# Kernel tuning notes

Measured on AMD Instinct MI355X. Metric: run time of the kernel, lower is better.

## Reference

```python
import jax, jax.numpy as jnp
import numpy as np

B, L, DIM, HID, DSSH, DSSN = 2, 4096, 1024, 4096, 512, 512


def _ln(x, w, b):
    # LayerNorm over last dim, eps=1e-5 (torch default)
    m = x.mean(-1, keepdims=True)
    v = ((x - m) ** 2).mean(-1, keepdims=True)
    return (x - m) * jax.lax.rsqrt(v + 1e-5) * w + b


def _dss(x, n2_w, n2_b, LR, LI, CR, CI, D):
    # x: [B, L, dss_hidden]
    Lseq = x.shape[-2]
    xn = _ln(x, n2_w, n2_b)
    Lam = (-jnp.exp(LR) + 1j * jnp.exp(LI)).astype(jnp.complex64)        # [N]
    t = jnp.arange(Lseq, dtype=jnp.float32)
    S = jnp.exp(Lam[:, None] * t[None, :])                               # [N, L]
    Cc = (CR + 1j * CI) * ((jnp.exp(Lam) - 1.0) / Lam)                   # [H, N]
    K = jnp.einsum('hn,nl->lh', Cc, S).real                              # [L, H]
    n2 = 2 * Lseq
    Kf = jnp.fft.rfft(K, n=n2, axis=-2)                                  # [L+1, H]
    uf = jnp.fft.rfft(xn, n=n2, axis=-2)                                 # [B, L+1, H]
    y = jnp.fft.irfft(uf * Kf, n=n2, axis=-2)[..., :Lseq, :]
    return y + D * xn


def setup_inputs() -> dict:
    key = jax.random.key(0)
    ks = jax.random.split(key, 12)
    s = lambda k, sh, sc=1.0: jax.random.normal(k, sh, jnp.float32) * sc
    return dict(
        idx=s(ks[0], (B, L, DIM)),
        n1_w=jnp.ones((DIM,), jnp.float32), n1_b=jnp.zeros((DIM,), jnp.float32),
        Wxg=s(ks[1], (DIM, HID), 0.02),
        Wdin=s(ks[2], (DIM, DSSH), 0.02),
        n2_w=jnp.ones((DSSH,), jnp.float32), n2_b=jnp.zeros((DSSH,), jnp.float32),
        LR=s(ks[3], (DSSN,)), LI=s(ks[4], (DSSN,)),
        CR=s(ks[5], (DSSH, DSSN), 0.1), CI=s(ks[6], (DSSH, DSSN), 0.1),
        D=s(ks[7], (DSSH,)),
        Wgate=s(ks[8], (DSSH, HID), 0.02),
        Wout=s(ks[9], (HID, DIM), 0.02), bout=jnp.zeros((DIM,), jnp.float32),
    )


def reference(idx, n1_w, n1_b, Wxg, Wdin, n2_w, n2_b, LR, LI, CR, CI, D, Wgate, Wout, bout):
    x = _ln(idx, n1_w, n1_b)
    xg = x @ Wxg                                            # [B, L, HID]
    d = _dss(x @ Wdin, n2_w, n2_b, LR, LI, CR, CI, D)       # [B, L, DSSH]
    g = d @ Wgate                                           # [B, L, HID]
    out = (g * xg) @ Wout + bout                            # dropout is identity in eval
    return out + idx
```

## Files before the change

### kernel.cpp

```cpp
#include <hip/hip_runtime.h>
#include <math.h>


typedef unsigned short u16;
typedef unsigned int u32;
typedef __attribute__((ext_vector_type(8))) __bf16 bf16x8;
typedef __attribute__((ext_vector_type(4))) float f32x4;
typedef __attribute__((ext_vector_type(4))) u32 u32x4;

__device__ __forceinline__ u16 f2bf(float f) {
  u32 u = __float_as_uint(f);
  u32 r = u + 0x7FFFu + ((u >> 16) & 1u);
  return (u16)(r >> 16);
}
__device__ __forceinline__ float bf2f(u16 h) { return __uint_as_float(((u32)h) << 16); }

__device__ __forceinline__ void trans_conv_body(
    int bid, const float* __restrict__ in, u16* __restrict__ out, int K, int N,
    float (*t)[33]) {
  int tx = threadIdx.x & 31, ty = threadIdx.x >> 5;
  int nb = N >> 5;
  int k0 = (bid / nb) << 5;
  int n0 = (bid % nb) << 5;
#pragma unroll
  for (int i = 0; i < 32; i += 8)
    t[ty + i][tx] = in[(size_t)(k0 + ty + i) * N + n0 + tx];
  __syncthreads();
#pragma unroll
  for (int i = 0; i < 32; i += 8)
    out[(size_t)(n0 + ty + i) * K + k0 + tx] = f2bf(t[tx][ty + i]);
}

__device__ __forceinline__ void ln1_body(
    int bid, const float* __restrict__ in, const float* __restrict__ gw,
    const float* __restrict__ gb, u16* __restrict__ outp, float* sbuf) {
  const int D = 1024;
  int tid = threadIdx.x;
  const float4* r4 = (const float4*)(in + (size_t)bid * D);
  float4 v = r4[tid];
  float s = v.x + v.y + v.z + v.w;
  float ss = fmaf(v.x, v.x, fmaf(v.y, v.y, fmaf(v.z, v.z, v.w * v.w)));
#pragma unroll
  for (int o = 32; o >= 1; o >>= 1) { s += __shfl_xor(s, o); ss += __shfl_xor(ss, o); }
  float* sa = sbuf;
  float* sb = sbuf + 8;
  if ((tid & 63) == 0) { sa[tid >> 6] = s; sb[tid >> 6] = ss; }
  __syncthreads();
  float S = sa[0] + sa[1] + sa[2] + sa[3];
  float SS = sb[0] + sb[1] + sb[2] + sb[3];
  float mean = S / (float)D;
  float var = SS / (float)D - mean * mean;
  float inv = rsqrtf(var + 1e-5f);
  float4 wv = ((const float4*)gw)[tid];
  float4 bv = ((const float4*)gb)[tid];
  ushort4 o;
  o.x = f2bf((v.x - mean) * inv * wv.x + bv.x);
  o.y = f2bf((v.y - mean) * inv * wv.y + bv.y);
  o.z = f2bf((v.z - mean) * inv * wv.z + bv.z);
  o.w = f2bf((v.w - mean) * inv * wv.w + bv.w);
  ((ushort4*)outp)[(size_t)bid * (D >> 2) + tid] = o;
}

__device__ __forceinline__ void kgen_c_body(
    int bid, const float* __restrict__ LR, const float* __restrict__ LI,
    const float* __restrict__ CR, const float* __restrict__ CI, u16* __restrict__ Ct) {
  int idx0 = bid * 256 + threadIdx.x;
  int h = idx0 >> 9, n = idx0 & 511;
  float eLR = expf(LR[n]), eLI = expf(LI[n]);
  float lre = -eLR, lim = eLI;
  float er = expf(lre);
  float c, s;
  sincosf(lim, &s, &c);
  float wr = er * c - 1.0f, wi = er * s;
  float den = lre * lre + lim * lim;
  float gr = (wr * lre + wi * lim) / den;
  float gi = (wi * lre - wr * lim) / den;
  float cr = CR[(size_t)h * 512 + n], ci = CI[(size_t)h * 512 + n];
  float ccr = cr * gr - ci * gi;
  float cci = cr * gi + ci * gr;
  Ct[(size_t)h * 1024 + n] = f2bf(ccr);
  Ct[(size_t)h * 1024 + 512 + n] = f2bf(-cci);
}

__device__ __forceinline__ void twfill_body(int bid, float4* __restrict__ twg4) {
  int j = bid * 256 + threadIdx.x;
  float t1 = -6.2831853071795864769f * (float)j / 8192.0f;
  float s1, c1, s2, c2;
  sincosf(t1, &s1, &c1);
  sincosf(2.0f * t1, &s2, &c2);
  twg4[j] = {c1, s1, c2, s2};
}

__device__ __forceinline__ void tab_body(
    int bid, const float* __restrict__ LR, const float* __restrict__ LI,
    double* __restrict__ aexp, double* __restrict__ fexp) {
  int n = bid * 256 + threadIdx.x;
  if (n < 512) {
    aexp[n] = exp((double)LR[n]);
    fexp[n] = exp((double)LI[n]) * 0.15915494309189533577;
  }
}

__device__ __forceinline__ void ln_stats_body(
    int bid, const u16* __restrict__ xdTb, float* __restrict__ meanv,
    float* __restrict__ invv, float* sbuf) {
  int lane = threadIdx.x & 63;
  int seg = threadIdx.x >> 6;
  int col = bid * 64 + lane;
  float s = 0.f, ss = 0.f;
  const u16* p = xdTb + (size_t)(seg * 128) * 8192 + col;
#pragma unroll 8
  for (int r = 0; r < 128; ++r) {
    float v = bf2f(p[(size_t)r * 8192]);
    s += v; ss = fmaf(v, v, ss);
  }
  float* sa = sbuf;
  float* sb = sbuf + 256;
  sa[seg * 64 + lane] = s; sb[seg * 64 + lane] = ss;
  __syncthreads();
  if (threadIdx.x < 64) {
    float S = sa[lane] + sa[64 + lane] + sa[128 + lane] + sa[192 + lane];
    float SS = sb[lane] + sb[64 + lane] + sb[128 + lane] + sb[192 + lane];
    float mean = S * (1.0f / 512.0f);
    float var = SS * (1.0f / 512.0f) - mean * mean;
    meanv[bid * 64 + lane] = mean;
    invv[bid * 64 + lane] = rsqrtf(var + 1e-5f);
  }
}

template <int MODE>
__device__ __forceinline__ void gemm128p_body(
    int bid0, int nwg, const u16* __restrict__ A, const u16* __restrict__ Bt,
    int M, int N, int K, float* Cf, u16* Cb,
    const float* __restrict__ bias, const float* __restrict__ res, u16* lds) {
  constexpr int BUF = 16384;
  const int tid = threadIdx.x;
  const int lane = tid & 63;
  const int w = tid >> 6;
  const int cpx = nwg >> 3;
  const int bid = (nwg & 7) ? bid0 : (bid0 & 7) * cpx + (bid0 >> 3);
  const int tiles_n = N >> 7;
  const int tm = (bid / tiles_n) << 7;
  const int tn = (bid % tiles_n) << 7;

  const int wm = w >> 1, wn = w & 1;
  const int lr = lane & 15;
  const int kq = lane >> 4;
  const int l7 = lane & 7;
  const int rsub = lane >> 3;
  const int sslot = (lane & 7) ^ rsub;
  const u16* gA = A + (size_t)(tm + w * 32 + rsub) * K + sslot * 8;
  const u16* gB = Bt + (size_t)(tn + w * 32 + rsub) * K + sslot * 8;
  auto ldsc = (__attribute__((address_space(3))) char*)lds;

#define STAGE128(kt, c)                                                                   \
  {                                                                                       \
    const size_t kof = (size_t)(kt) << 6;                                                 \
    _Pragma("unroll") for (int i = 0; i < 4; ++i) {                                       \
      u32 da = (u32)((c)*BUF + (w * 32 + i * 8) * 64) * 2u;                               \
      __builtin_amdgcn_global_load_lds(                                                   \
          (const __attribute__((address_space(1))) void*)(gA + (size_t)(i * 8) * K + kof),\
          (__attribute__((address_space(3))) void*)(ldsc + da), 16, 0, 0);                \
      __builtin_amdgcn_global_load_lds(                                                   \
          (const __attribute__((address_space(1))) void*)(gB + (size_t)(i * 8) * K + kof),\
          (__attribute__((address_space(3))) void*)(ldsc + da + 16384), 16, 0, 0);        \
    }                                                                                     \
  }

  f32x4 acc[4][4] = {};
  const int NT = K >> 6;

  STAGE128(0, 0);
  asm volatile("s_waitcnt vmcnt(0)" ::: "memory");
  __builtin_amdgcn_s_barrier();
  __builtin_amdgcn_sched_barrier(0);

  int cur = 0;
  for (int kt = 0; kt < NT; ++kt) {
    if (kt + 1 < NT) STAGE128(kt + 1, cur ^ 1);
    const u32 ab = (u32)cur * BUF;
#pragma unroll
    for (int ks = 0; ks < 2; ++ks) {
      const int slp = ((((ks << 2) | kq)) ^ l7) << 3;
      bf16x8 af[4], bv[4];
#pragma unroll
      for (int mi = 0; mi < 4; ++mi) {
        int ra = wm * 64 + mi * 16 + lr;
        af[mi] = *(const bf16x8*)&lds[ab + ra * 64 + slp];
      }
#pragma unroll
      for (int ni = 0; ni < 4; ++ni) {
        int rb = wn * 64 + ni * 16 + lr;
        bv[ni] = *(const bf16x8*)&lds[ab + 8192 + rb * 64 + slp];
      }
      __builtin_amdgcn_s_setprio(1);
#pragma unroll
      for (int mi = 0; mi < 4; ++mi)
#pragma unroll
        for (int ni = 0; ni < 4; ++ni)
          acc[mi][ni] = __builtin_amdgcn_mfma_f32_16x16x32_bf16(af[mi], bv[ni], acc[mi][ni], 0, 0, 0);
      __builtin_amdgcn_s_setprio(0);
    }
    asm volatile("s_waitcnt vmcnt(0)" ::: "memory");
    __builtin_amdgcn_s_barrier();
    __builtin_amdgcn_sched_barrier(0);
    cur ^= 1;
  }
#undef STAGE128

  float* lf = (float*)lds + w * (16 * 68);
  const int er = lane >> 2;
  const int ec = (lane & 3) << 4;
  const int gcol = tn + wn * 64 + ec;
#pragma unroll
  for (int mi = 0; mi < 4; ++mi) {
#pragma unroll
    for (int ni = 0; ni < 4; ++ni)
#pragma unroll
      for (int j = 0; j < 4; ++j)
        lf[(kq * 4 + j) * 68 + ni * 16 + lr] = acc[mi][ni][j];
    float v[16];
#pragma unroll
    for (int q = 0; q < 4; ++q)
      *(f32x4*)&v[q * 4] = *(const f32x4*)&lf[er * 68 + ec + q * 4];
    const int gr = tm + wm * 64 + mi * 16 + er;
    if (MODE == 3) {
      const float* rr = res + (size_t)gr * N + gcol;
      const float* br = bias + gcol;
      float* orr = Cf + (size_t)gr * N + gcol;
#pragma unroll
      for (int q = 0; q < 4; ++q) {
        f32x4 rv = *(const f32x4*)(rr + q * 4);
        f32x4 bv4 = *(const f32x4*)(br + q * 4);
        f32x4 ov;
        ov[0] = v[q * 4 + 0] + bv4[0] + rv[0];
        ov[1] = v[q * 4 + 1] + bv4[1] + rv[1];
        ov[2] = v[q * 4 + 2] + bv4[2] + rv[2];
        ov[3] = v[q * 4 + 3] + bv4[3] + rv[3];
        *(f32x4*)(orr + q * 4) = ov;
      }
    } else {
      u32 pk[8];
#pragma unroll
      for (int e = 0; e < 8; ++e)
        pk[e] = (u32)f2bf(v[2 * e]) | ((u32)f2bf(v[2 * e + 1]) << 16);
      u16* orr = Cb + (size_t)gr * N + gcol;
      *(u32x4*)orr = u32x4{pk[0], pk[1], pk[2], pk[3]};
      *(u32x4*)(orr + 8) = u32x4{pk[4], pk[5], pk[6], pk[7]};
    }
  }
}


__global__ __launch_bounds__(256) void mega1(
    const float* __restrict__ idxf, const float* __restrict__ n1w, const float* __restrict__ n1b,
    const float* __restrict__ Wxg, const float* __restrict__ Wdin,
    const float* __restrict__ Wgate, const float* __restrict__ Wout,
    u16* __restrict__ Wxg_t, u16* __restrict__ Wdin_t,
    u16* __restrict__ Wgate_t, u16* __restrict__ Wout_t,
    u16* __restrict__ xbf, float4* __restrict__ twg4,
    const float* __restrict__ LR, const float* __restrict__ LI,
    const float* __restrict__ CR, const float* __restrict__ CI,
    u16* __restrict__ Ct, double* __restrict__ aexp, double* __restrict__ fexp) {
  __shared__ __align__(16) char smem[4352];
  int b = (int)blockIdx.x;
  if (b < 8192) { ln1_body(b, idxf, n1w, n1b, xbf, (float*)smem); return; }
  b -= 8192;
  if (b < 4096) { trans_conv_body(b, Wxg, Wxg_t, 1024, 4096, (float(*)[33])smem); return; }
  b -= 4096;
  if (b < 4096) { trans_conv_body(b, Wout, Wout_t, 4096, 1024, (float(*)[33])smem); return; }
  b -= 4096;
  if (b < 2048) { trans_conv_body(b, Wgate, Wgate_t, 512, 4096, (float(*)[33])smem); return; }
  b -= 2048;
  if (b < 512) { trans_conv_body(b, Wdin, Wdin_t, 1024, 512, (float(*)[33])smem); return; }
  b -= 512;
  if (b < 1024) { kgen_c_body(b, LR, LI, CR, CI, Ct); return; }
  b -= 1024;
  if (b < 8) { twfill_body(b, twg4); return; }
  b -= 8;
  tab_body(b, LR, LI, aexp, fexp);
}

__global__ __launch_bounds__(256) void kgen_s2(
    const double* __restrict__ aexp, const double* __restrict__ fexp,
    u16* __restrict__ SRSI) {
  int idx0 = (int)blockIdx.x * 256 + threadIdx.x;
  int l = idx0 >> 10;
  int kk = idx0 & 1023;
  int n = kk & 511;
  double fl = fexp[n] * (double)l;
  float rev = (float)(fl - floor(fl));
  float tri = (kk < 512) ? __builtin_amdgcn_cosf(rev) : __builtin_amdgcn_sinf(rev);
  float al = (float)aexp[n] * (float)l;
  SRSI[idx0] = f2bf(expf(-al) * tri);
}

template <int MODE>
__global__ __launch_bounds__(256, 2) void gemm128p(
    const u16* __restrict__ A, const u16* __restrict__ Bt,
    int M, int N, int K,
    float* Cf, u16* Cb,
    const float* __restrict__ bias, const float* __restrict__ res) {
  __shared__ __align__(16) u16 lds[2 * 16384];
  gemm128p_body<MODE>((int)blockIdx.x, (int)gridDim.x, A, Bt, M, N, K, Cf, Cb, bias, res, lds);
}

__global__ __launch_bounds__(256, 2) void l3mix(
    const u16* __restrict__ Ct, const u16* __restrict__ SRSI, u16* __restrict__ KTb,
    const u16* __restrict__ xdTb, float* __restrict__ meanv, float* __restrict__ invv) {
  __shared__ __align__(16) u16 lds[2 * 16384];
  int b = (int)blockIdx.x;
  if (b < 128) {
    gemm128p_body<1>(b, 128, Ct, SRSI, 512, 4096, 1024, nullptr, KTb, nullptr, nullptr, lds);
  } else {
    ln_stats_body(b - 128, xdTb, meanv, invv, (float*)lds);
  }
}

__global__ __launch_bounds__(256) void trans_bf(
    const u16* __restrict__ in, u16* __restrict__ out, int R, int C) {
  __shared__ u16 t[32][34];
  int tx = threadIdx.x & 31, ty = threadIdx.x >> 5;
  int nb = C >> 5;
  int r0 = (blockIdx.x / nb) << 5;
  int c0 = (blockIdx.x % nb) << 5;
#pragma unroll
  for (int i = 0; i < 32; i += 8)
    t[ty + i][tx] = in[(size_t)(r0 + ty + i) * C + c0 + tx];
  __syncthreads();
#pragma unroll
  for (int i = 0; i < 32; i += 8)
    out[(size_t)(c0 + ty + i) * R + r0 + tx] = t[tx][ty + i];
}

__global__ __launch_bounds__(256, 2) void gemm_fuse2(
    const u16* __restrict__ A1, const u16* __restrict__ B1t, int K1,
    const u16* __restrict__ A2, const u16* __restrict__ B2t, int K2,
    int M, int N, u16* __restrict__ Cb) {
  constexpr int BUF = 16384;
  __shared__ __align__(16) u16 lds[2 * BUF];
  const int tid = threadIdx.x;
  const int lane = tid & 63;
  const int w = tid >> 6;
  const int nwg = (int)gridDim.x;
  const int cpx = nwg >> 3;
  const int bid = (nwg & 7) ? (int)blockIdx.x
                            : ((int)blockIdx.x & 7) * cpx + ((int)blockIdx.x >> 3);
  const int tiles_n = N >> 7;
  const int tm = (bid / tiles_n) << 7;
  const int tn = (bid % tiles_n) << 7;

  const int wm = w >> 1, wn = w & 1;
  const int lr = lane & 15;
  const int kq = lane >> 4;
  const int l7 = lane & 7;
  const int rsub = lane >> 3;
  const int sslot = (lane & 7) ^ rsub;
  auto ldsc = (__attribute__((address_space(3))) char*)lds;

  f32x4 acc1[4][4] = {};
  f32x4 acc2[4][4] = {};

#define STAGEF(gA, gB, K, kt, c)                                                          \
  {                                                                                       \
    const size_t kof = (size_t)(kt) << 6;                                                 \
    _Pragma("unroll") for (int i = 0; i < 4; ++i) {                                       \
      u32 da = (u32)((c)*BUF + (w * 32 + i * 8) * 64) * 2u;                               \
      __builtin_amdgcn_global_load_lds(                                                   \
          (const __attribute__((address_space(1))) void*)((gA) + (size_t)(i * 8) * (K) + kof), \
          (__attribute__((address_space(3))) void*)(ldsc + da), 16, 0, 0);                \
      __builtin_amdgcn_global_load_lds(                                                   \
          (const __attribute__((address_space(1))) void*)((gB) + (size_t)(i * 8) * (K) + kof), \
          (__attribute__((address_space(3))) void*)(ldsc + da + 16384), 16, 0, 0);        \
    }                                                                                     \
  }

#define KLOOP(gA, gB, K, ACC)                                                             \
  {                                                                                       \
    const int NT = (K) >> 6;                                                              \
    STAGEF(gA, gB, K, 0, 0);                                                              \
    asm volatile("s_waitcnt vmcnt(0)" ::: "memory");                                      \
    __builtin_amdgcn_s_barrier();                                                         \
    __builtin_amdgcn_sched_barrier(0);                                                    \
    int cur = 0;                                                                          \
    for (int kt = 0; kt < NT; ++kt) {                                                     \
      if (kt + 1 < NT) STAGEF(gA, gB, K, kt + 1, cur ^ 1);                                \
      const u32 ab = (u32)cur * BUF;                                                      \
      _Pragma("unroll") for (int ks = 0; ks < 2; ++ks) {                                  \
        const int slp = ((((ks << 2) | kq)) ^ l7) << 3;                                   \
        bf16x8 af[4], bv[4];                                                              \
        _Pragma("unroll") for (int mi = 0; mi < 4; ++mi) {                                \
          int ra = wm * 64 + mi * 16 + lr;                                                \
          af[mi] = *(const bf16x8*)&lds[ab + ra * 64 + slp];                              \
        }                                                                                 \
        _Pragma("unroll") for (int ni = 0; ni < 4; ++ni) {                                \
          int rb = wn * 64 + ni * 16 + lr;                                                \
          bv[ni] = *(const bf16x8*)&lds[ab + 8192 + rb * 64 + slp];                       \
        }                                                                                 \
        __builtin_amdgcn_s_setprio(1);                                                    \
        _Pragma("unroll") for (int mi = 0; mi < 4; ++mi)                                  \
          _Pragma("unroll") for (int ni = 0; ni < 4; ++ni)                                \
            ACC[mi][ni] = __builtin_amdgcn_mfma_f32_16x16x32_bf16(af[mi], bv[ni], ACC[mi][ni], 0, 0, 0); \
        __builtin_amdgcn_s_setprio(0);                                                    \
      }                                                                                   \
      asm volatile("s_waitcnt vmcnt(0)" ::: "memory");                                    \
      __builtin_amdgcn_s_barrier();                                                       \
      __builtin_amdgcn_sched_barrier(0);                                                  \
      cur ^= 1;                                                                           \
    }                                                                                     \
  }

  {
    const u16* gA = A1 + (size_t)(tm + w * 32 + rsub) * K1 + sslot * 8;
    const u16* gB = B1t + (size_t)(tn + w * 32 + rsub) * K1 + sslot * 8;
    KLOOP(gA, gB, K1, acc1);
  }
  {
    const u16* gA = A2 + (size_t)(tm + w * 32 + rsub) * K2 + sslot * 8;
    const u16* gB = B2t + (size_t)(tn + w * 32 + rsub) * K2 + sslot * 8;
    KLOOP(gA, gB, K2, acc2);
  }
#undef KLOOP
#undef STAGEF

#pragma unroll
  for (int mi = 0; mi < 4; ++mi)
#pragma unroll
    for (int ni = 0; ni < 4; ++ni)
#pragma unroll
      for (int j = 0; j < 4; ++j)
        acc1[mi][ni][j] *= acc2[mi][ni][j];

  float* lf = (float*)lds + w * (16 * 68);
  const int er = lane >> 2;
  const int ec = (lane & 3) << 4;
  const int gcol = tn + wn * 64 + ec;
#pragma unroll
  for (int mi = 0; mi < 4; ++mi) {
#pragma unroll
    for (int ni = 0; ni < 4; ++ni)
#pragma unroll
      for (int j = 0; j < 4; ++j)
        lf[(kq * 4 + j) * 68 + ni * 16 + lr] = acc1[mi][ni][j];
    float v[16];
#pragma unroll
    for (int q = 0; q < 4; ++q)
      *(f32x4*)&v[q * 4] = *(const f32x4*)&lf[er * 68 + ec + q * 4];
    const int gr = tm + wm * 64 + mi * 16 + er;
    u32 pk[8];
#pragma unroll
    for (int e = 0; e < 8; ++e)
      pk[e] = (u32)f2bf(v[2 * e]) | ((u32)f2bf(v[2 * e + 1]) << 16);
    u16* orr = Cb + (size_t)gr * N + gcol;
    *(u32x4*)orr = u32x4{pk[0], pk[1], pk[2], pk[3]};
    *(u32x4*)(orr + 8) = u32x4{pk[4], pk[5], pk[6], pk[7]};
  }
}

struct C2 { float x, y; };
__device__ __forceinline__ C2 cadd(C2 a, C2 b) { return {a.x + b.x, a.y + b.y}; }
__device__ __forceinline__ C2 csub(C2 a, C2 b) { return {a.x - b.x, a.y - b.y}; }
__device__ __forceinline__ C2 cmul(C2 a, C2 b) {
  return {a.x * b.x - a.y * b.y, a.x * b.y + a.y * b.x};
}
__device__ __forceinline__ C2 cmulni(C2 a) { return {a.y, -a.x}; }

__device__ __forceinline__ int swz(int a) {
  return a ^ ((a >> 7) & 15) ^ ((a >> 11) & 3) ^ ((a >> 2) & 8) ^ ((a >> 3) & 2) ^ ((a >> 4) & 4);
}

#define BR13(x) ((int)(__brev((u32)(x)) >> 19))
#define RS 0.70710678118654752f

__device__ __forceinline__ void dif4(C2& a, C2& b, C2& c, C2& d, float4 wv) {
  C2 w = {wv.x, wv.y}, wm = {wv.y, -wv.x}, w2 = {wv.z, wv.w};
  C2 a1 = cadd(a, c);
  C2 c1 = cmul(csub(a, c), w);
  C2 b1 = cadd(b, d);
  C2 d1 = cmul(csub(b, d), wm);
  a = cadd(a1, b1);
  b = cmul(csub(a1, b1), w2);
  c = cadd(c1, d1);
  d = cmul(csub(c1, d1), w2);
}
__device__ __forceinline__ void dit4(C2& a, C2& b, C2& c, C2& d, float4 wv) {
  C2 w = {wv.x, wv.y}, wm = {wv.y, -wv.x}, wa = {wv.z, wv.w};
  C2 t = cmul(wa, b);
  C2 a1 = cadd(a, t), b1 = csub(a, t);
  C2 u = cmul(wa, d);
  C2 c1 = cadd(c, u), d1 = csub(c, u);
  C2 v = cmul(w, c1);
  C2 xx = cmul(wm, d1);
  a = cadd(a1, v);
  c = csub(a1, v);
  b = cadd(b1, xx);
  d = csub(b1, xx);
}

template <int L>
__device__ __forceinline__ void dif16(C2* z, int tid, const float4* __restrict__ twg4) {
  const int Q = 1 << (L - 2);
  const int pos2 = tid & (Q - 1);
  const int i0 = ((tid >> (L - 2)) << (L + 2)) | pos2;
  int ad[16]; C2 x[16];
#pragma unroll
  for (int k = 0; k < 16; ++k) { ad[k] = swz(i0 + k * Q); x[k] = z[ad[k]]; }
#pragma unroll
  for (int r = 0; r < 4; ++r)
    dif4(x[r], x[r + 4], x[r + 8], x[r + 12], twg4[(pos2 + r * Q) << (11 - L)]);
  {
    float4 wv2 = twg4[pos2 << (13 - L)];
#pragma unroll
    for (int m = 0; m < 4; ++m)
      dif4(x[4 * m], x[4 * m + 1], x[4 * m + 2], x[4 * m + 3], wv2);
  }
#pragma unroll
  for (int k = 0; k < 16; ++k) z[ad[k]] = x[k];
}
template <int L>
__device__ __forceinline__ void dit16(C2* z, int tid, const float4* __restrict__ twg4) {
  const int Q = 1 << (L - 2);
  const int pos2 = tid & (Q - 1);
  const int i0 = ((tid >> (L - 2)) << (L + 2)) | pos2;
  int ad[16]; C2 x[16];
#pragma unroll
  for (int k = 0; k < 16; ++k) { ad[k] = swz(i0 + k * Q); x[k] = z[ad[k]]; }
  {
    float4 wv2 = twg4[pos2 << (13 - L)];
#pragma unroll
    for (int m = 0; m < 4; ++m)
      dit4(x[4 * m], x[4 * m + 1], x[4 * m + 2], x[4 * m + 3], wv2);
  }
#pragma unroll
  for (int r = 0; r < 4; ++r)
    dit4(x[r], x[r + 4], x[r + 8], x[r + 12], twg4[(pos2 + r * Q) << (11 - L)]);
#pragma unroll
  for (int k = 0; k < 16; ++k) z[ad[k]] = x[k];
}

template <int LOGM>
__device__ __forceinline__ void dif_pass(C2* z, int tid, const float4* __restrict__ twg4) {
  const int M4 = 1 << LOGM;
#pragma unroll
  for (int j = 0; j < 4; ++j) {
    int b = tid + j * 512;
    int pos = b & (M4 - 1);
    int i0 = ((b >> LOGM) << (LOGM + 2)) | pos;
    int ia = swz(i0), ib = swz(i0 + M4), ic = swz(i0 + 2 * M4), id = swz(i0 + 3 * M4);
    C2 a = z[ia], bb = z[ib], c = z[ic], d = z[id];
    float4 wv = twg4[pos << (11 - LOGM)];
    dif4(a, bb, c, d, wv);
    z[ia] = a; z[ib] = bb; z[ic] = c; z[id] = d;
  }
}

template <int LOGM>
__device__ __forceinline__ void dit_pass(C2* z, int tid, const float4* __restrict__ twg4) {
  const int M4 = 1 << LOGM;
#pragma unroll
  for (int j = 0; j < 4; ++j) {
    int b = tid + j * 512;
    int pos = b & (M4 - 1);
    int i0 = ((b >> LOGM) << (LOGM + 2)) | pos;
    int ia = swz(i0), ib = swz(i0 + M4), ic = swz(i0 + 2 * M4), id = swz(i0 + 3 * M4);
    C2 a = z[ia], bb = z[ib], c = z[ic], d = z[id];
    float4 wv = twg4[pos << (11 - LOGM)];
    dit4(a, bb, c, d, wv);
    z[ia] = a; z[ib] = bb; z[ic] = c; z[id] = d;
  }
}

__device__ __forceinline__ void dif_r8(C2* z, int tid) {
#pragma unroll
  for (int j = 0; j < 2; ++j) {
    int base = (tid + j * 512) << 3;
    int ad[8]; C2 x[8];
#pragma unroll
    for (int e = 0; e < 8; ++e) { ad[e] = swz(base + e); x[e] = z[ad[e]]; }
    C2 t;
    t = csub(x[0], x[4]); x[0] = cadd(x[0], x[4]); x[4] = t;
    t = csub(x[1], x[5]); x[1] = cadd(x[1], x[5]); x[5] = cmul(t, {RS, -RS});
    t = csub(x[2], x[6]); x[2] = cadd(x[2], x[6]); x[6] = cmulni(t);
    t = csub(x[3], x[7]); x[3] = cadd(x[3], x[7]); x[7] = cmul(t, {-RS, -RS});
    t = csub(x[0], x[2]); x[0] = cadd(x[0], x[2]); x[2] = t;
    t = csub(x[1], x[3]); x[1] = cadd(x[1], x[3]); x[3] = cmulni(t);
    t = csub(x[4], x[6]); x[4] = cadd(x[4], x[6]); x[6] = t;
    t = csub(x[5], x[7]); x[5] = cadd(x[5], x[7]); x[7] = cmulni(t);
    t = csub(x[0], x[1]); x[0] = cadd(x[0], x[1]); x[1] = t;
    t = csub(x[2], x[3]); x[2] = cadd(x[2], x[3]); x[3] = t;
    t = csub(x[4], x[5]); x[4] = cadd(x[4], x[5]); x[5] = t;
    t = csub(x[6], x[7]); x[6] = cadd(x[6], x[7]); x[7] = t;
#pragma unroll
    for (int e = 0; e < 8; ++e) z[ad[e]] = x[e];
  }
}

__device__ __forceinline__ void r8_fused(C2* z, int tid, const u32* __restrict__ kfr) {
#pragma unroll
  for (int j = 0; j < 2; ++j) {
    int base = (tid + j * 512) << 3;
    int ad[8]; C2 x[8];
#pragma unroll
    for (int e = 0; e < 8; ++e) { ad[e] = swz(base + e); x[e] = z[ad[e]]; }
    u32x4 k0 = *(const u32x4*)(kfr + base);
    u32x4 k1 = *(const u32x4*)(kfr + base + 4);
    u32 kw[8] = {k0[0], k0[1], k0[2], k0[3], k1[0], k1[1], k1[2], k1[3]};
    C2 t;
    t = csub(x[0], x[4]); x[0] = cadd(x[0], x[4]); x[4] = t;
    t = csub(x[1], x[5]); x[1] = cadd(x[1], x[5]); x[5] = cmul(t, {RS, -RS});
    t = csub(x[2], x[6]); x[2] = cadd(x[2], x[6]); x[6] = cmulni(t);
    t = csub(x[3], x[7]); x[3] = cadd(x[3], x[7]); x[7] = cmul(t, {-RS, -RS});
    t = csub(x[0], x[2]); x[0] = cadd(x[0], x[2]); x[2] = t;
    t = csub(x[1], x[3]); x[1] = cadd(x[1], x[3]); x[3] = cmulni(t);
    t = csub(x[4], x[6]); x[4] = cadd(x[4], x[6]); x[6] = t;
    t = csub(x[5], x[7]); x[5] = cadd(x[5], x[7]); x[7] = cmulni(t);
    t = csub(x[0], x[1]); x[0] = cadd(x[0], x[1]); x[1] = t;
    t = csub(x[2], x[3]); x[2] = cadd(x[2], x[3]); x[3] = t;
    t = csub(x[4], x[5]); x[4] = cadd(x[4], x[5]); x[5] = t;
    t = csub(x[6], x[7]); x[6] = cadd(x[6], x[7]); x[7] = t;
#pragma unroll
    for (int e = 0; e < 8; ++e) {
      C2 kf = {bf2f((u16)(kw[e] & 0xffffu)), bf2f((u16)(kw[e] >> 16))};
      C2 pr = cmul(x[e], kf);
      x[e] = {pr.x, -pr.y};
    }
    t = x[1]; x[1] = csub(x[0], t); x[0] = cadd(x[0], t);
    t = x[3]; x[3] = csub(x[2], t); x[2] = cadd(x[2], t);
    t = x[5]; x[5] = csub(x[4], t); x[4] = cadd(x[4], t);
    t = x[7]; x[7] = csub(x[6], t); x[6] = cadd(x[6], t);
    t = x[2];          x[2] = csub(x[0], t); x[0] = cadd(x[0], t);
    t = cmulni(x[3]);  x[3] = csub(x[1], t); x[1] = cadd(x[1], t);
    t = x[6];          x[6] = csub(x[4], t); x[4] = cadd(x[4], t);
    t = cmulni(x[7]);  x[7] = csub(x[5], t); x[5] = cadd(x[5], t);
    t = x[4];                    x[4] = csub(x[0], t); x[0] = cadd(x[0], t);
    t = cmul(x[5], {RS, -RS});   x[5] = csub(x[1], t); x[1] = cadd(x[1], t);
    t = cmulni(x[6]);            x[6] = csub(x[2], t); x[2] = cadd(x[2], t);
    t = cmul(x[7], {-RS, -RS});  x[7] = csub(x[3], t); x[3] = cadd(x[3], t);
#pragma unroll
    for (int e = 0; e < 8; ++e) z[ad[e]] = x[e];
  }
}

__global__ __launch_bounds__(512) void kfft2(
    const u16* __restrict__ KTb, const float4* __restrict__ twg4,
    u32* __restrict__ Kfb) {
  __shared__ C2 z[8192];
  const int g = blockIdx.x;
  const int t = threadIdx.x;
  const u16* k0r = KTb + ((size_t)(2 * g) << 12);
  const u16* k1r = KTb + ((size_t)(2 * g + 1) << 12);

  C2 x[16];
#pragma unroll
  for (int k = 0; k < 8; ++k) {
    int l = t + k * 512;
    x[k] = {bf2f(k0r[l]), bf2f(k1r[l])};
  }
#pragma unroll
  for (int k = 8; k < 16; ++k) x[k] = {0.f, 0.f};
#pragma unroll
  for (int r = 0; r < 4; ++r)
    dif4(x[r], x[r + 4], x[r + 8], x[r + 12], twg4[t + r * 512]);
  {
    float4 wv2 = twg4[t << 2];
#pragma unroll
    for (int m = 0; m < 4; ++m)
      dif4(x[4 * m], x[4 * m + 1], x[4 * m + 2], x[4 * m + 3], wv2);
  }
#pragma unroll
  for (int k = 0; k < 16; ++k) z[swz(t + k * 512)] = x[k];
  __syncthreads();

  dif16<7>(z, t, twg4);   __syncthreads();
  dif_pass<3>(z, t, twg4); __syncthreads();
  dif_r8(z, t);            __syncthreads();

  u32* o0 = Kfb + ((size_t)(2 * g) << 13);
  u32* o1 = Kfb + ((size_t)(2 * g + 1) << 13);
#pragma unroll
  for (int it = 0; it < 16; ++it) {
    int p = t + it * 512;
    int k = BR13(p);
    int km = (8192 - k) & 8191;
    int p2 = BR13(km);
    C2 Zk = z[swz(p)], Zm = z[swz(p2)];
    float f0r = 0.5f * (Zk.x + Zm.x), f0i = 0.5f * (Zk.y - Zm.y);
    float f1r = 0.5f * (Zk.y + Zm.y), f1i = 0.5f * (Zm.x - Zk.x);
    o0[p] = (u32)f2bf(f0r) | ((u32)f2bf(f0i) << 16);
    o1[p] = (u32)f2bf(f1r) | ((u32)f2bf(f1i) << 16);
  }
}

__global__ __launch_bounds__(512) void fft_conv4(
    const u16* __restrict__ xdTb, const u32* __restrict__ Kfb,
    const float* __restrict__ meanv, const float* __restrict__ invv,
    const float* __restrict__ n2w, const float* __restrict__ n2b,
    const float* __restrict__ Dv, const float4* __restrict__ twg4,
    u16* __restrict__ dT) {
  __shared__ C2 z[8192];
  const int h = blockIdx.x;
  const int t = threadIdx.x;
  const u16* xr = xdTb + ((size_t)h << 13);
  const float w2h = n2w[h], b2h = n2b[h], Dh = Dv[h];

  float xn0r[8], xn1r[8];
  C2 x[16];
#pragma unroll
  for (int k = 0; k < 8; ++k) {
    int l = t + k * 512;
    float x0 = bf2f(xr[l]);
    float x1 = bf2f(xr[4096 + l]);
    xn0r[k] = (x0 - meanv[l]) * invv[l] * w2h + b2h;
    xn1r[k] = (x1 - meanv[4096 + l]) * invv[4096 + l] * w2h + b2h;
    x[k] = {xn0r[k], xn1r[k]};
  }
#pragma unroll
  for (int k = 8; k < 16; ++k) x[k] = {0.f, 0.f};
#pragma unroll
  for (int r = 0; r < 4; ++r)
    dif4(x[r], x[r + 4], x[r + 8], x[r + 12], twg4[t + r * 512]);
  {
    float4 wv2 = twg4[t << 2];
#pragma unroll
    for (int m = 0; m < 4; ++m)
      dif4(x[4 * m], x[4 * m + 1], x[4 * m + 2], x[4 * m + 3], wv2);
  }
#pragma unroll
  for (int k = 0; k < 16; ++k) z[swz(t + k * 512)] = x[k];
  __syncthreads();

  dif16<7>(z, t, twg4);    __syncthreads();
  dif_pass<3>(z, t, twg4);  __syncthreads();
  r8_fused(z, t, Kfb + ((size_t)h << 13)); __syncthreads();
  dit_pass<3>(z, t, twg4);  __syncthreads();
  dit16<7>(z, t, twg4);     __syncthreads();

#pragma unroll
  for (int k = 0; k < 16; ++k) x[k] = z[swz(t + k * 512)];
  {
    float4 wv2 = twg4[t << 2];
#pragma unroll
    for (int m = 0; m < 4; ++m)
      dit4(x[4 * m], x[4 * m + 1], x[4 * m + 2], x[4 * m + 3], wv2);
  }
  const float sc = 1.0f / 8192.0f;
  u16* drow = dT + ((size_t)h << 13);
#pragma unroll
  for (int r = 0; r < 4; ++r) {
    float4 wv = twg4[t + r * 512];
    C2 w = {wv.x, wv.y}, wm = {wv.y, -wv.x}, wa = {wv.z, wv.w};
    C2 a = x[r], bb = x[r + 4], c = x[r + 8], d = x[r + 12];
    C2 tt = cmul(wa, bb);
    C2 a1 = cadd(a, tt), b1 = csub(a, tt);
    C2 u = cmul(wa, d);
    C2 c1 = cadd(c, u), d1 = csub(c, u);
    C2 olo = cadd(a1, cmul(w, c1));
    C2 ohi = cadd(b1, cmul(wm, d1));
    int l0 = t + r * 512;
    int l1 = t + (r + 4) * 512;
    drow[l0] = f2bf(fmaf(Dh, xn0r[r], olo.x * sc));
    drow[4096 + l0] = f2bf(fmaf(Dh, xn1r[r], -olo.y * sc));
    drow[l1] = f2bf(fmaf(Dh, xn0r[r + 4], ohi.x * sc));
    drow[4096 + l1] = f2bf(fmaf(Dh, xn1r[r + 4], -ohi.y * sc));
  }
}

extern "C" void kernel_launch(void* const* d_in, const int* in_sizes, int n_in,
                              void* d_out, int out_size, void* d_ws, size_t ws_size,
                              hipStream_t stream) {
  (void)in_sizes; (void)n_in; (void)out_size; (void)ws_size;
  const float* idx  = (const float*)d_in[0];
  const float* n1w  = (const float*)d_in[1];
  const float* n1b  = (const float*)d_in[2];
  const float* Wxg  = (const float*)d_in[3];
  const float* Wdin = (const float*)d_in[4];
  const float* n2w  = (const float*)d_in[5];
  const float* n2b  = (const float*)d_in[6];
  const float* LR   = (const float*)d_in[7];
  const float* LI   = (const float*)d_in[8];
  const float* CR   = (const float*)d_in[9];
  const float* CI   = (const float*)d_in[10];
  const float* Dv   = (const float*)d_in[11];
  const float* Wgate= (const float*)d_in[12];
  const float* Wout = (const float*)d_in[13];
  const float* bout = (const float*)d_in[14];
  float* out = (float*)d_out;

  const int L = 4096, DIM = 1024, HID = 4096, H = 512;
  const int M = 8192;

  char* p = (char*)d_ws;
  auto alloc = [&](size_t bytes) { char* q = p; p += (bytes + 255) & ~(size_t)255; return q; };
  u16* Wxg_t   = (u16*)alloc((size_t)HID * DIM * 2);
  u16* Wdin_t  = (u16*)alloc((size_t)H * DIM * 2);
  u16* Wgate_t = (u16*)alloc((size_t)HID * H * 2);
  u16* Wout_t  = (u16*)alloc((size_t)DIM * HID * 2);
  u16* xbf     = (u16*)alloc((size_t)M * DIM * 2);
  u16* ebuf    = (u16*)alloc((size_t)M * HID * 2);
  u16* xdTb    = (u16*)alloc((size_t)H * M * 2);
  float* meanv = (float*)alloc((size_t)M * 4);
  float* invv  = (float*)alloc((size_t)M * 4);
  u16* SRSI    = (u16*)alloc((size_t)L * 1024 * 2);
  u16* Ct      = (u16*)alloc((size_t)H * 1024 * 2);
  u16* KTb     = (u16*)alloc((size_t)H * L * 2);
  u16* dTm     = (u16*)alloc((size_t)H * M * 2);
  u16* dbuf    = (u16*)alloc((size_t)M * H * 2);
  float4* twg4 = (float4*)alloc((size_t)2048 * 16);
  u32* Kfb     = (u32*)alloc((size_t)H * M * 4);
  double* aexp = (double*)alloc((size_t)512 * 8);
  double* fexp = (double*)alloc((size_t)512 * 8);

  mega1<<<dim3(8192 + 4096 + 4096 + 2048 + 512 + 1024 + 8 + 2), 256, 0, stream>>>(
      idx, n1w, n1b, Wxg, Wdin, Wgate, Wout,
      Wxg_t, Wdin_t, Wgate_t, Wout_t, xbf, twg4, LR, LI, CR, CI, Ct, aexp, fexp);
  kgen_s2<<<dim3(L * 1024 / 256), 256, 0, stream>>>(aexp, fexp, SRSI);
  gemm128p<1><<<dim3((H / 128) * (M / 128)), 256, 0, stream>>>(
      Wdin_t, xbf, H, M, DIM, nullptr, xdTb, nullptr, nullptr);
  l3mix<<<dim3(256), 256, 0, stream>>>(Ct, SRSI, KTb, xdTb, meanv, invv);
  kfft2<<<dim3(H / 2), 512, 0, stream>>>(KTb, twg4, Kfb);
  fft_conv4<<<dim3(H), 512, 0, stream>>>(xdTb, Kfb, meanv, invv, n2w, n2b, Dv, twg4, dTm);
  trans_bf<<<dim3((H / 32) * (M / 32)), 256, 0, stream>>>(dTm, dbuf, H, M);
  gemm_fuse2<<<dim3((M / 128) * (HID / 128)), 256, 0, stream>>>(
      xbf, Wxg_t, DIM, dbuf, Wgate_t, H, M, HID, ebuf);
  gemm128p<3><<<dim3((M / 128) * (DIM / 128)), 256, 0, stream>>>(
      ebuf, Wout_t, M, DIM, HID, out, nullptr, bout, idx);
}
```

Measured before the change: 311.6 us.

## Replace double-buffered BK=64 GEMM mainloop with 4-stage BK=32 LDS ring

All GEMM mainloops (gemm128s, l3mix GEMM part, gemm_fuse2) now use a 4-deep ring of BK=32 stages loaded with global_load_lds. Partial vmcnt waits keep up to three stages in flight instead of draining all loads every iteration. The LDS swizzle is redone for 32-element rows. Each iteration now has two barriers and less MFMA work per sync, which adds synchronisation overhead in exchange for deeper memory latency hiding.

```diff
diff --git a/kernel.cpp b/kernel.cpp
--- a/kernel.cpp
+++ b/kernel.cpp
@@ -128,12 +128,61 @@
   }
 }
 
+
+#define RING_STAGE(AP, BP, K, kt)                                                         \
+  {                                                                                       \
+    const u32 cb = (u32)((kt) & 3) * 16384u;                                              \
+    const size_t kof = (size_t)(kt) << 5;                                                 \
+    _Pragma("unroll") for (int i = 0; i < 2; ++i) {                                       \
+      u32 da = cb + (u32)(i * 64 + wv16) * 64u;                                           \
+      __builtin_amdgcn_global_load_lds(                                                   \
+          (const __attribute__((address_space(1))) void*)((AP) + (size_t)(i * 64) * (K) + kof), \
+          (__attribute__((address_space(3))) void*)(ldsc + da), 16, 0, 0);                \
+      __builtin_amdgcn_global_load_lds(                                                   \
+          (const __attribute__((address_space(1))) void*)((BP) + (size_t)(i * 64) * (K) + kof), \
+          (__attribute__((address_space(3))) void*)(ldsc + da + 8192), 16, 0, 0);         \
+    }                                                                                     \
+  }
+
+#define RING_LOOP(Aptr, Bptr, K, ACC)                                                     \
+  {                                                                                       \
+    const int NT = (K) >> 5;                                                              \
+    RING_STAGE(Aptr, Bptr, K, 0);                                                         \
+    RING_STAGE(Aptr, Bptr, K, 1);                                                         \
+    RING_STAGE(Aptr, Bptr, K, 2);                                                         \
+    asm volatile("s_waitcnt vmcnt(8)" ::: "memory");                                      \
+    __builtin_amdgcn_s_barrier();                                                         \
+    for (int kt = 0; kt < NT; ++kt) {                                                     \
+      if (kt + 3 < NT) RING_STAGE(Aptr, Bptr, K, kt + 3);                                 \
+      if (kt + 3 < NT)      asm volatile("s_waitcnt vmcnt(12)" ::: "memory");             \
+      else if (kt + 2 < NT) asm volatile("s_waitcnt vmcnt(8)" ::: "memory");              \
+      else if (kt + 1 < NT) asm volatile("s_waitcnt vmcnt(4)" ::: "memory");              \
+      else                  asm volatile("s_waitcnt vmcnt(0)" ::: "memory");              \
+      __builtin_amdgcn_s_barrier();                                                       \
+      const u32 ab = (u32)(kt & 3) * 8192u;                                               \
+      bf16x8 af[4], bv[4];                                                                \
+      _Pragma("unroll") for (int mi = 0; mi < 4; ++mi) {                                  \
+        int ra = wm * 64 + mi * 16 + lr;                                                  \
+        af[mi] = *(const bf16x8*)&lds[ab + ra * 32 + slp];                                \
+      }                                                                                   \
+      _Pragma("unroll") for (int ni = 0; ni < 4; ++ni) {                                  \
+        int rb = wn * 64 + ni * 16 + lr;                                                  \
+        bv[ni] = *(const bf16x8*)&lds[ab + 4096 + rb * 32 + slp];                         \
+      }                                                                                   \
+      __builtin_amdgcn_s_setprio(1);                                                      \
+      _Pragma("unroll") for (int mi = 0; mi < 4; ++mi)                                    \
+        _Pragma("unroll") for (int ni = 0; ni < 4; ++ni)                                  \
+          ACC[mi][ni] = __builtin_amdgcn_mfma_f32_16x16x32_bf16(af[mi], bv[ni], ACC[mi][ni], 0, 0, 0); \
+      __builtin_amdgcn_s_setprio(0);                                                      \
+      __builtin_amdgcn_s_barrier();                                                      \
+    }                                                                                     \
+  }
+
 template <int MODE>
-__device__ __forceinline__ void gemm128p_body(
+__device__ __forceinline__ void gemm128s_body(
     int bid0, int nwg, const u16* __restrict__ A, const u16* __restrict__ Bt,
     int M, int N, int K, float* Cf, u16* Cb,
     const float* __restrict__ bias, const float* __restrict__ res, u16* lds) {
-  constexpr int BUF = 16384;
   const int tid = threadIdx.x;
   const int lane = tid & 63;
   const int w = tid >> 6;
@@ -146,67 +195,16 @@
   const int wm = w >> 1, wn = w & 1;
   const int lr = lane & 15;
   const int kq = lane >> 4;
-  const int l7 = lane & 7;
-  const int rsub = lane >> 3;
-  const int sslot = (lane & 7) ^ rsub;
-  const u16* gA = A + (size_t)(tm + w * 32 + rsub) * K + sslot * 8;
-  const u16* gB = Bt + (size_t)(tn + w * 32 + rsub) * K + sslot * 8;
+  const int slp = ((kq ^ (lr & 3)) << 3);
+  const int wv16 = w * 16;
+  const int srow = wv16 + (lane >> 2);
+  const int sslot = (lane & 3) ^ ((lane >> 2) & 3);
+  const u16* gA = A + (size_t)(tm + srow) * K + sslot * 8;
+  const u16* gB = Bt + (size_t)(tn + srow) * K + sslot * 8;
   auto ldsc = (__attribute__((address_space(3))) char*)lds;
 
-#define STAGE128(kt, c)                                                                   \
-  {                                                                                       \
-    const size_t kof = (size_t)(kt) << 6;                                                 \
-    _Pragma("unroll") for (int i = 0; i < 4; ++i) {                                       \
-      u32 da = (u32)((c)*BUF + (w * 32 + i * 8) * 64) * 2u;                               \
-      __builtin_amdgcn_global_load_lds(                                                   \
-          (const __attribute__((address_space(1))) void*)(gA + (size_t)(i * 8) * K + kof),\
-          (__attribute__((address_space(3))) void*)(ldsc + da), 16, 0, 0);                \
-      __builtin_amdgcn_global_load_lds(                                                   \
-          (const __attribute__((address_space(1))) void*)(gB + (size_t)(i * 8) * K + kof),\
-          (__attribute__((address_space(3))) void*)(ldsc + da + 16384), 16, 0, 0);        \
-    }                                                                                     \
-  }
-
   f32x4 acc[4][4] = {};
-  const int NT = K >> 6;
-
-  STAGE128(0, 0);
-  asm volatile("s_waitcnt vmcnt(0)" ::: "memory");
-  __builtin_amdgcn_s_barrier();
-  __builtin_amdgcn_sched_barrier(0);
-
-  int cur = 0;
-  for (int kt = 0; kt < NT; ++kt) {
-    if (kt + 1 < NT) STAGE128(kt + 1, cur ^ 1);
-    const u32 ab = (u32)cur * BUF;
-#pragma unroll
-    for (int ks = 0; ks < 2; ++ks) {
-      const int slp = ((((ks << 2) | kq)) ^ l7) << 3;
-      bf16x8 af[4], bv[4];
-#pragma unroll
-      for (int mi = 0; mi < 4; ++mi) {
-        int ra = wm * 64 + mi * 16 + lr;
-        af[mi] = *(const bf16x8*)&lds[ab + ra * 64 + slp];
-      }
-#pragma unroll
-      for (int ni = 0; ni < 4; ++ni) {
-        int rb = wn * 64 + ni * 16 + lr;
-        bv[ni] = *(const bf16x8*)&lds[ab + 8192 + rb * 64 + slp];
-      }
-      __builtin_amdgcn_s_setprio(1);
-#pragma unroll
-      for (int mi = 0; mi < 4; ++mi)
-#pragma unroll
-        for (int ni = 0; ni < 4; ++ni)
-          acc[mi][ni] = __builtin_amdgcn_mfma_f32_16x16x32_bf16(af[mi], bv[ni], acc[mi][ni], 0, 0, 0);
-      __builtin_amdgcn_s_setprio(0);
-    }
-    asm volatile("s_waitcnt vmcnt(0)" ::: "memory");
-    __builtin_amdgcn_s_barrier();
-    __builtin_amdgcn_sched_barrier(0);
-    cur ^= 1;
-  }
-#undef STAGE128
+  RING_LOOP(gA, gB, K, acc);
 
   float* lf = (float*)lds + w * (16 * 68);
   const int er = lane >> 2;
@@ -250,7 +248,6 @@
     }
   }
 }
-
 
 __global__ __launch_bounds__(256) void mega1(
     const float* __restrict__ idxf, const float* __restrict__ n1w, const float* __restrict__ n1b,
@@ -296,22 +293,22 @@
 }
 
 template <int MODE>
-__global__ __launch_bounds__(256, 2) void gemm128p(
+__global__ __launch_bounds__(256, 2) void gemm128s(
     const u16* __restrict__ A, const u16* __restrict__ Bt,
     int M, int N, int K,
     float* Cf, u16* Cb,
     const float* __restrict__ bias, const float* __restrict__ res) {
-  __shared__ __align__(16) u16 lds[2 * 16384];
-  gemm128p_body<MODE>((int)blockIdx.x, (int)gridDim.x, A, Bt, M, N, K, Cf, Cb, bias, res, lds);
+  __shared__ __align__(16) u16 lds[32768];
+  gemm128s_body<MODE>((int)blockIdx.x, (int)gridDim.x, A, Bt, M, N, K, Cf, Cb, bias, res, lds);
 }
 
 __global__ __launch_bounds__(256, 2) void l3mix(
     const u16* __restrict__ Ct, const u16* __restrict__ SRSI, u16* __restrict__ KTb,
     const u16* __restrict__ xdTb, float* __restrict__ meanv, float* __restrict__ invv) {
-  __shared__ __align__(16) u16 lds[2 * 16384];
+  __shared__ __align__(16) u16 lds[32768];
   int b = (int)blockIdx.x;
   if (b < 128) {
-    gemm128p_body<1>(b, 128, Ct, SRSI, 512, 4096, 1024, nullptr, KTb, nullptr, nullptr, lds);
+    gemm128s_body<1>(b, 128, Ct, SRSI, 512, 4096, 1024, nullptr, KTb, nullptr, nullptr, lds);
   } else {
     ln_stats_body(b - 128, xdTb, meanv, invv, (float*)lds);
   }
@@ -337,8 +334,7 @@
     const u16* __restrict__ A1, const u16* __restrict__ B1t, int K1,
     const u16* __restrict__ A2, const u16* __restrict__ B2t, int K2,
     int M, int N, u16* __restrict__ Cb) {
-  constexpr int BUF = 16384;
-  __shared__ __align__(16) u16 lds[2 * BUF];
+  __shared__ __align__(16) u16 lds[32768];
   const int tid = threadIdx.x;
   const int lane = tid & 63;
   const int w = tid >> 6;
@@ -353,75 +349,25 @@
   const int wm = w >> 1, wn = w & 1;
   const int lr = lane & 15;
   const int kq = lane >> 4;
-  const int l7 = lane & 7;
-  const int rsub = lane >> 3;
-  const int sslot = (lane & 7) ^ rsub;
+  const int slp = ((kq ^ (lr & 3)) << 3);
+  const int wv16 = w * 16;
+  const int srow = wv16 + (lane >> 2);
+  const int sslot = (lane & 3) ^ ((lane >> 2) & 3);
   auto ldsc = (__attribute__((address_space(3))) char*)lds;
 
   f32x4 acc1[4][4] = {};
   f32x4 acc2[4][4] = {};
 
-#define STAGEF(gA, gB, K, kt, c)                                                          \
-  {                                                                                       \
-    const size_t kof = (size_t)(kt) << 6;                                                 \
-    _Pragma("unroll") for (int i = 0; i < 4; ++i) {                                       \
-      u32 da = (u32)((c)*BUF + (w * 32 + i * 8) * 64) * 2u;                               \
-      __builtin_amdgcn_global_load_lds(                                                   \
-          (const __attribute__((address_space(1))) void*)((gA) + (size_t)(i * 8) * (K) + kof), \
-          (__attribute__((address_space(3))) void*)(ldsc + da), 16, 0, 0);                \
-      __builtin_amdgcn_global_load_lds(                                                   \
-          (const __attribute__((address_space(1))) void*)((gB) + (size_t)(i * 8) * (K) + kof), \
-          (__attribute__((address_space(3))) void*)(ldsc + da + 16384), 16, 0, 0);        \
-    }                                                                                     \
-  }
-
-#define KLOOP(gA, gB, K, ACC)                                                             \
-  {                                                                                       \
-    const int NT = (K) >> 6;                                                              \
-    STAGEF(gA, gB, K, 0, 0);                                                              \
-    asm volatile("s_waitcnt vmcnt(0)" ::: "memory");                                      \
-    __builtin_amdgcn_s_barrier();                                                         \
-    __builtin_amdgcn_sched_barrier(0);                                                    \
-    int cur = 0;                                                                          \
-    for (int kt = 0; kt < NT; ++kt) {                                                     \
-      if (kt + 1 < NT) STAGEF(gA, gB, K, kt + 1, cur ^ 1);                                \
-      const u32 ab = (u32)cur * BUF;                                                      \
-      _Pragma("unroll") for (int ks = 0; ks < 2; ++ks) {                                  \
-        const int slp = ((((ks << 2) | kq)) ^ l7) << 3;                                   \
-        bf16x8 af[4], bv[4];                                                              \
-        _Pragma("unroll") for (int mi = 0; mi < 4; ++mi) {                                \
-          int ra = wm * 64 + mi * 16 + lr;                                                \
-          af[mi] = *(const bf16x8*)&lds[ab + ra * 64 + slp];                              \
-        }                                                                                 \
-        _Pragma("unroll") for (int ni = 0; ni < 4; ++ni) {                                \
-          int rb = wn * 64 + ni * 16 + lr;                                                \
-          bv[ni] = *(const bf16x8*)&lds[ab + 8192 + rb * 64 + slp];                       \
-        }                                                                                 \
-        __builtin_amdgcn_s_setprio(1);                                                    \
-        _Pragma("unroll") for (int mi = 0; mi < 4; ++mi)                                  \
-          _Pragma("unroll") for (int ni = 0; ni < 4; ++ni)                                \
-            ACC[mi][ni] = __builtin_amdgcn_mfma_f32_16x16x32_bf16(af[mi], bv[ni], ACC[mi][ni], 0, 0, 0); \
-        __builtin_amdgcn_s_setprio(0);                                                    \
-      }                                                                                   \
-      asm volatile("s_waitcnt vmcnt(0)" ::: "memory");                                    \
-      __builtin_amdgcn_s_barrier();                                                       \
-      __builtin_amdgcn_sched_barrier(0);                                                  \
-      cur ^= 1;                                                                           \
-    }                                                                                     \
-  }
-
   {
-    const u16* gA = A1 + (size_t)(tm + w * 32 + rsub) * K1 + sslot * 8;
-    const u16* gB = B1t + (size_t)(tn + w * 32 + rsub) * K1 + sslot * 8;
-    KLOOP(gA, gB, K1, acc1);
+    const u16* gA = A1 + (size_t)(tm + srow) * K1 + sslot * 8;
+    const u16* gB = B1t + (size_t)(tn + srow) * K1 + sslot * 8;
+    RING_LOOP(gA, gB, K1, acc1);
   }
   {
-    const u16* gA = A2 + (size_t)(tm + w * 32 + rsub) * K2 + sslot * 8;
-    const u16* gB = B2t + (size_t)(tn + w * 32 + rsub) * K2 + sslot * 8;
-    KLOOP(gA, gB, K2, acc2);
-  }
-#undef KLOOP
-#undef STAGEF
+    const u16* gA = A2 + (size_t)(tm + srow) * K2 + sslot * 8;
+    const u16* gB = B2t + (size_t)(tn + srow) * K2 + sslot * 8;
+    RING_LOOP(gA, gB, K2, acc2);
+  }
 
 #pragma unroll
   for (int mi = 0; mi < 4; ++mi)
@@ -814,7 +760,7 @@
       idx, n1w, n1b, Wxg, Wdin, Wgate, Wout,
       Wxg_t, Wdin_t, Wgate_t, Wout_t, xbf, twg4, LR, LI, CR, CI, Ct, aexp, fexp);
   kgen_s2<<<dim3(L * 1024 / 256), 256, 0, stream>>>(aexp, fexp, SRSI);
-  gemm128p<1><<<dim3((H / 128) * (M / 128)), 256, 0, stream>>>(
+  gemm128s<1><<<dim3((H / 128) * (M / 128)), 256, 0, stream>>>(
       Wdin_t, xbf, H, M, DIM, nullptr, xdTb, nullptr, nullptr);
   l3mix<<<dim3(256), 256, 0, stream>>>(Ct, SRSI, KTb, xdTb, meanv, invv);
   kfft2<<<dim3(H / 2), 512, 0, stream>>>(KTb, twg4, Kfb);
@@ -822,6 +768,6 @@
   trans_bf<<<dim3((H / 32) * (M / 32)), 256, 0, stream>>>(dTm, dbuf, H, M);
   gemm_fuse2<<<dim3((M / 128) * (HID / 128)), 256, 0, stream>>>(
       xbf, Wxg_t, DIM, dbuf, Wgate_t, H, M, HID, ebuf);
-  gemm128p<3><<<dim3((M / 128) * (DIM / 128)), 256, 0, stream>>>(
+  gemm128s<3><<<dim3((M / 128) * (DIM / 128)), 256, 0, stream>>>(
       ebuf, Wout_t, M, DIM, HID, out, nullptr, bout, idx);
 }
```

After: 332.1 us. 1.07x slower.
